# Optimization experiments

Measured on AMD Instinct MI355X. Metric: run time of the kernel, lower is better.

The kernel has to match this reference:

```python
import jax, jax.numpy as jnp
import numpy as np


def setup_inputs() -> dict:
    key = jax.random.key(0)
    ks = jax.random.split(key, 4)
    B, T, D, U = 32, 1024, 1024, 1024
    x = jax.random.normal(ks[0], (B, T, D), dtype=jnp.float32)
    W = jax.random.normal(ks[1], (D, 4 * U), dtype=jnp.float32) * (1.0 / np.sqrt(D))
    b = jnp.zeros((4 * U,), dtype=jnp.float32)
    Vr = jax.random.normal(ks[2], (U,), dtype=jnp.float32) * 0.1
    Vf = jax.random.normal(ks[3], (U,), dtype=jnp.float32) * 0.1
    h0 = jnp.zeros((B, U), dtype=jnp.float32)
    c0 = jnp.zeros((B, U), dtype=jnp.float32)
    return {"x": x, "h0": h0, "c0": c0, "W": W, "b": b, "Vr": Vr, "Vf": Vf}


def _sru(x, h0, c0, W, b, Vr, Vf):
    B, T, D = x.shape
    U = Vr.shape[0]
    # Batched matmul across all timesteps, then sequential elementwise scan.
    g = jnp.einsum('btd,dk->btk', x, W) + b            # [B, T, 4U]
    g = jnp.moveaxis(g, 1, 0)                          # [T, B, 4U]
    g1, g2, g3, g4 = jnp.split(g, 4, axis=-1)          # each [T, B, U]

    def step(c_, gs):
        a1, a2, a3, a4 = gs
        f = jax.nn.sigmoid(a1 + Vf * c_)
        c = f * c_ + (1.0 - f) * a2
        r = jax.nn.sigmoid(a3 + Vr * c_)
        h = r * c + (1.0 - r) * a4
        return c, h

    c_last, hs = jax.lax.scan(step, c0, (g1, g2, g3, g4))
    return jnp.moveaxis(hs, 0, 1)                      # [B, T, U]


def reference(x, h0, c0, W, b, Vr, Vf):
    return _sru(x, h0, c0, W, b, Vr, Vf)
```

## Files before the change

### kernel.cpp

```cpp
#include <hip/hip_runtime.h>
#include <cstdint>
#include <cstddef>

typedef short short8 __attribute__((ext_vector_type(8)));
typedef short s16x4 __attribute__((ext_vector_type(4)));
typedef float f32x4 __attribute__((ext_vector_type(4)));

typedef const __attribute__((address_space(1))) void* gas_ptr;
typedef __attribute__((address_space(3))) void* las_ptr;

__device__ __forceinline__ unsigned short f2bf(float f) {
    unsigned int u = __float_as_uint(f);
    u += 0x7fffu + ((u >> 16) & 1u);
    return (unsigned short)(u >> 16);
}
__device__ __forceinline__ float bf2f(unsigned short s) {
    return __uint_as_float(((unsigned int)s) << 16);
}
__device__ __forceinline__ float sigmoid_f(float z) {
    return __builtin_amdgcn_rcpf(1.0f + __expf(-z));
}
__device__ __forceinline__ void async_copy16(const void* gp, void* lp) {
    __builtin_amdgcn_global_load_lds((gas_ptr)gp, (las_ptr)lp, 16, 0, 0);
}

__global__ __launch_bounds__(256) void cvt_x_kernel(const float* __restrict__ in,
                                                    unsigned short* __restrict__ out) {
    size_t i = ((size_t)blockIdx.x * 256 + threadIdx.x) * 8;
    float4 v0 = *(const float4*)(in + i);
    float4 v1 = *(const float4*)(in + i + 4);
    short8 o;
    o[0]=(short)f2bf(v0.x); o[1]=(short)f2bf(v0.y); o[2]=(short)f2bf(v0.z); o[3]=(short)f2bf(v0.w);
    o[4]=(short)f2bf(v1.x); o[5]=(short)f2bf(v1.y); o[6]=(short)f2bf(v1.z); o[7]=(short)f2bf(v1.w);
    *(short8*)(out + i) = o;
}

__global__ __launch_bounds__(256) void cvt_w_kernel(const float* __restrict__ W,
                                                    unsigned short* __restrict__ Wt) {
    __shared__ unsigned short tile[64][65];
    int bk = blockIdx.x >> 6, bn = blockIdx.x & 63;
    int k0 = bk * 64, n0 = bn * 64;
    int t = threadIdx.x;
    int cr = t >> 6;
    int cc = t & 63;
#pragma unroll
    for (int i = 0; i < 16; ++i) {
        int row = i * 4 + cr;
        tile[row][cc] = f2bf(W[(size_t)(k0 + row) * 4096 + n0 + cc]);
    }
    __syncthreads();
#pragma unroll
    for (int i = 0; i < 16; ++i) {
        int nrow = i * 4 + cr;
        Wt[(size_t)(n0 + nrow) * 1024 + k0 + cc] = tile[cc][nrow];
    }
}

__global__ __launch_bounds__(256, 2) void gemm_kernel(const unsigned short* __restrict__ A,
                                                      const unsigned short* __restrict__ Bt,
                                                      const float* __restrict__ bias,
                                                      unsigned short* __restrict__ gT) {
    __shared__ __align__(16) unsigned short As[128 * 64];
    __shared__ __align__(16) unsigned short Bs[128 * 64];

    int bid = blockIdx.x;
    int band = bid >> 8;
    int r = bid & 255;
    int mt = band * 8 + (r >> 5);
    int nt = r & 31;
    int m0 = mt * 128, n0 = nt * 128;

    int tidx = threadIdx.x;
    int lane = tidx & 63, wv = tidx >> 6;
    int wm = wv >> 1, wn = wv & 1;
    int l15 = lane & 15, quad = lane >> 4;

    f32x4 acc[4][4] = {};

    for (int k0 = 0; k0 < 1024; k0 += 64) {
        __syncthreads();
#pragma unroll
        for (int i = 0; i < 4; ++i) {
            int ci = (wv * 4 + i) * 64 + lane;
            int row = ci >> 3, cc = ci & 7;
            int sc = (cc ^ (row & 7)) << 3;
            const unsigned short* ga = A + (size_t)(m0 + row) * 1024 + k0 + sc;
            async_copy16(ga, (char*)As + (wv * 4 + i) * 1024);
            const unsigned short* gb = Bt + (size_t)(n0 + row) * 1024 + k0 + sc;
            async_copy16(gb, (char*)Bs + (wv * 4 + i) * 1024);
        }
        __syncthreads();
#pragma unroll
        for (int kt = 0; kt < 2; ++kt) {
            short8 af[4], bf[4];
#pragma unroll
            for (int mt2 = 0; mt2 < 4; ++mt2) {
                int row = wm * 64 + mt2 * 16 + l15;
                int kc = kt * 4 + quad;
                af[mt2] = *(const short8*)((const char*)As + row * 128 + ((kc ^ (row & 7)) << 4));
            }
#pragma unroll
            for (int nt2 = 0; nt2 < 4; ++nt2) {
                int rown = wn * 64 + nt2 * 16 + l15;
                int kc = kt * 4 + quad;
                bf[nt2] = *(const short8*)((const char*)Bs + rown * 128 + ((kc ^ (rown & 7)) << 4));
            }
#pragma unroll
            for (int mt2 = 0; mt2 < 4; ++mt2)
#pragma unroll
                for (int nt2 = 0; nt2 < 4; ++nt2)
                    acc[mt2][nt2] = __builtin_amdgcn_mfma_f32_16x16x32_bf16(
                        af[mt2], bf[nt2], acc[mt2][nt2], 0, 0, 0);
        }
    }

#pragma unroll
    for (int mt2 = 0; mt2 < 4; ++mt2) {
        int mbase = m0 + wm * 64 + mt2 * 16 + quad * 4;
        int b_ = mbase >> 10, t_ = mbase & 1023;
#pragma unroll
        for (int nt2 = 0; nt2 < 4; ++nt2) {
            int n = n0 + wn * 64 + nt2 * 16 + l15;
            int gate = n >> 10, u = n & 1023;
            float bv = bias[n];
            s16x4 pk;
            pk[0] = (short)f2bf(acc[mt2][nt2][0] + bv);
            pk[1] = (short)f2bf(acc[mt2][nt2][1] + bv);
            pk[2] = (short)f2bf(acc[mt2][nt2][2] + bv);
            pk[3] = (short)f2bf(acc[mt2][nt2][3] + bv);
            size_t off = ((((size_t)(t_ >> 3) * 32 + (size_t)b_) * 4 + (size_t)gate) << 13)
                         + ((size_t)u << 3) + (size_t)(t_ & 7);
            *(s16x4*)(gT + off) = pk;
        }
    }
}

__global__ __launch_bounds__(128) void scan_kernel(const unsigned short* __restrict__ gT,
                                                   const float* __restrict__ c0,
                                                   const float* __restrict__ Vr,
                                                   const float* __restrict__ Vf,
                                                   float* __restrict__ h) {
    __shared__ __align__(16) unsigned short sbuf[8 * 2048];

    const int NT = 128;
    const int D = 8;
    int blk = blockIdx.x;
    int b = blk >> 4;
    int u0 = (blk & 15) << 6;
    int tid = threadIdx.x;
    int wv = tid >> 6;
    int lane = tid & 63;

    if (wv == 0) {
        size_t base = ((size_t)b * 4) * 8192 + ((size_t)(u0 + lane) << 3);
        const unsigned short* pg0 = gT + base;
        const unsigned short* pg1 = pg0 + 8192;
        const unsigned short* pg2 = pg1 + 8192;
        const unsigned short* pg3 = pg2 + 8192;
#pragma unroll
        for (int g = 0; g < D - 1; ++g) {
            char* ld = (char*)sbuf + (g & 7) * 4096;
            size_t o = (size_t)g << 20;
            async_copy16(pg0 + o, ld);
            async_copy16(pg1 + o, ld + 1024);
            async_copy16(pg2 + o, ld + 2048);
            async_copy16(pg3 + o, ld + 3072);
        }
        for (int j = 0; j < NT; ++j) {
            if (j < NT - (D - 2)) {
                asm volatile("s_waitcnt vmcnt(24)" ::: "memory");
            } else {
                asm volatile("s_waitcnt vmcnt(0)" ::: "memory");
            }
            __builtin_amdgcn_s_barrier();
            int g = j + D - 1;
            if (g < NT) {
                char* ld = (char*)sbuf + (g & 7) * 4096;
                size_t o = (size_t)g << 20;
                async_copy16(pg0 + o, ld);
                async_copy16(pg1 + o, ld + 1024);
                async_copy16(pg2 + o, ld + 2048);
                async_copy16(pg3 + o, ld + 3072);
            }
        }
    } else {
        int u = u0 + lane;
        float c = c0[(b << 10) + u];
        float vf = Vf[u], vr = Vr[u];
        float* hb = h + ((size_t)b << 20) + u;
        const unsigned short* ls = sbuf + (size_t)lane * 8;
        for (int j = 0; j < NT; ++j) {
            __builtin_amdgcn_s_barrier();
            asm volatile("" ::: "memory");
            int so = (j & 7) * 2048;
            short8 a1 = *(const short8*)(ls + so);
            short8 a2 = *(const short8*)(ls + so + 512);
            short8 a3 = *(const short8*)(ls + so + 1024);
            short8 a4 = *(const short8*)(ls + so + 1536);
            int t0 = j * 8;
#pragma unroll
            for (int i = 0; i < 8; ++i) {
                float x1 = bf2f((unsigned short)a1[i]);
                float x2 = bf2f((unsigned short)a2[i]);
                float x3 = bf2f((unsigned short)a3[i]);
                float x4 = bf2f((unsigned short)a4[i]);
                float f  = sigmoid_f(x1 + vf * c);
                float cn = fmaf(f, c - x2, x2);
                float rr = sigmoid_f(x3 + vr * c);
                float hv = fmaf(rr, cn - x4, x4);
                c = cn;
                hb[(size_t)(t0 + i) << 10] = hv;
            }
        }
    }
}

extern "C" void kernel_launch(void* const* d_in, const int* in_sizes, int n_in,
                              void* d_out, int out_size, void* d_ws, size_t ws_size,
                              hipStream_t stream) {
    const float* x  = (const float*)d_in[0];
    const float* c0 = (const float*)d_in[2];
    const float* W  = (const float*)d_in[3];
    const float* b  = (const float*)d_in[4];
    const float* Vr = (const float*)d_in[5];
    const float* Vf = (const float*)d_in[6];
    float* h = (float*)d_out;

    char* ws = (char*)d_ws;
    unsigned short* xb = (unsigned short*)ws;
    unsigned short* wt = (unsigned short*)(ws + (size_t)67108864);
    unsigned short* gT = (unsigned short*)(ws + (size_t)75497472);

    cvt_x_kernel<<<16384, 256, 0, stream>>>(x, xb);
    cvt_w_kernel<<<1024, 256, 0, stream>>>(W, wt);
    gemm_kernel<<<8192, 256, 0, stream>>>(xb, wt, b, gT);
    scan_kernel<<<512, 128, 0, stream>>>(gT, c0, Vr, Vf, h);
}
```

Before: 550.3 us.

## Split scan into serial c-checkpoint pass and parallel h-recompute pass

The sequential scan now runs only the cell-state recurrence, reading just the forget and candidate gates, and stores a checkpoint of c every 128 timesteps into reused workspace. A second kernel launches one thread per (chunk, batch, unit), starts from those checkpoints, and recomputes c alongside h for its 128-step chunk, streaming all four gates directly from global memory with register prefetch. This moves the h computation and output writes off the latency-bound serial path and spreads them across many more threads. The cost is an extra launch, rereading gates 1 and 2, and the serial pass stopping after 112 of 128 blocks because the last chunk needs no checkpoint.

```diff
diff --git a/kernel.cpp b/kernel.cpp
--- a/kernel.cpp
+++ b/kernel.cpp
@@ -135,14 +135,13 @@
     }
 }
 
-__global__ __launch_bounds__(128) void scan_kernel(const unsigned short* __restrict__ gT,
-                                                   const float* __restrict__ c0,
-                                                   const float* __restrict__ Vr,
-                                                   const float* __restrict__ Vf,
-                                                   float* __restrict__ h) {
-    __shared__ __align__(16) unsigned short sbuf[8 * 2048];
-
-    const int NT = 128;
+__global__ __launch_bounds__(128) void scan_c_kernel(const unsigned short* __restrict__ gT,
+                                                     const float* __restrict__ c0,
+                                                     const float* __restrict__ Vf,
+                                                     float* __restrict__ cB) {
+    __shared__ __align__(16) unsigned short sbuf[8 * 1024];
+
+    const int NT = 112;
     const int D = 8;
     int blk = blockIdx.x;
     int b = blk >> 4;
@@ -155,62 +154,97 @@
         size_t base = ((size_t)b * 4) * 8192 + ((size_t)(u0 + lane) << 3);
         const unsigned short* pg0 = gT + base;
         const unsigned short* pg1 = pg0 + 8192;
-        const unsigned short* pg2 = pg1 + 8192;
-        const unsigned short* pg3 = pg2 + 8192;
 #pragma unroll
         for (int g = 0; g < D - 1; ++g) {
-            char* ld = (char*)sbuf + (g & 7) * 4096;
+            char* ld = (char*)sbuf + (g & 7) * 2048;
             size_t o = (size_t)g << 20;
             async_copy16(pg0 + o, ld);
             async_copy16(pg1 + o, ld + 1024);
-            async_copy16(pg2 + o, ld + 2048);
-            async_copy16(pg3 + o, ld + 3072);
         }
         for (int j = 0; j < NT; ++j) {
             if (j < NT - (D - 2)) {
-                asm volatile("s_waitcnt vmcnt(24)" ::: "memory");
+                asm volatile("s_waitcnt vmcnt(12)" ::: "memory");
             } else {
                 asm volatile("s_waitcnt vmcnt(0)" ::: "memory");
             }
             __builtin_amdgcn_s_barrier();
             int g = j + D - 1;
             if (g < NT) {
-                char* ld = (char*)sbuf + (g & 7) * 4096;
+                char* ld = (char*)sbuf + (g & 7) * 2048;
                 size_t o = (size_t)g << 20;
                 async_copy16(pg0 + o, ld);
                 async_copy16(pg1 + o, ld + 1024);
-                async_copy16(pg2 + o, ld + 2048);
-                async_copy16(pg3 + o, ld + 3072);
             }
         }
     } else {
         int u = u0 + lane;
         float c = c0[(b << 10) + u];
-        float vf = Vf[u], vr = Vr[u];
-        float* hb = h + ((size_t)b << 20) + u;
+        float vf = Vf[u];
         const unsigned short* ls = sbuf + (size_t)lane * 8;
         for (int j = 0; j < NT; ++j) {
             __builtin_amdgcn_s_barrier();
             asm volatile("" ::: "memory");
-            int so = (j & 7) * 2048;
+            int so = (j & 7) * 1024;
             short8 a1 = *(const short8*)(ls + so);
             short8 a2 = *(const short8*)(ls + so + 512);
-            short8 a3 = *(const short8*)(ls + so + 1024);
-            short8 a4 = *(const short8*)(ls + so + 1536);
-            int t0 = j * 8;
 #pragma unroll
             for (int i = 0; i < 8; ++i) {
                 float x1 = bf2f((unsigned short)a1[i]);
                 float x2 = bf2f((unsigned short)a2[i]);
-                float x3 = bf2f((unsigned short)a3[i]);
-                float x4 = bf2f((unsigned short)a4[i]);
                 float f  = sigmoid_f(x1 + vf * c);
-                float cn = fmaf(f, c - x2, x2);
-                float rr = sigmoid_f(x3 + vr * c);
-                float hv = fmaf(rr, cn - x4, x4);
-                c = cn;
-                hb[(size_t)(t0 + i) << 10] = hv;
-            }
+                c = fmaf(f, c - x2, x2);
+            }
+            if ((j & 15) == 15) {
+                cB[((size_t)(j >> 4) << 15) + (size_t)(b << 10) + u] = c;
+            }
+        }
+    }
+}
+
+__global__ __launch_bounds__(256) void scan_h_kernel(const unsigned short* __restrict__ gT,
+                                                     const float* __restrict__ c0,
+                                                     const float* __restrict__ cB,
+                                                     const float* __restrict__ Vr,
+                                                     const float* __restrict__ Vf,
+                                                     float* __restrict__ h) {
+    int idx = blockIdx.x * 256 + threadIdx.x;
+    int u = idx & 1023;
+    int rb = idx >> 10;
+    int r = rb >> 5, b = rb & 31;
+    float vf = Vf[u], vr = Vr[u];
+    float c = (r == 0) ? c0[(b << 10) + u]
+                       : cB[((size_t)(r - 1) << 15) + (size_t)(b << 10) + u];
+    const unsigned short* base = gT + ((size_t)b * 4) * 8192 + ((size_t)u << 3);
+    float* hb = h + ((size_t)b << 20) + u;
+    int tb0 = r << 4;
+
+    const unsigned short* p0 = base + ((size_t)tb0 << 20);
+    short8 n1 = *(const short8*)(p0);
+    short8 n2 = *(const short8*)(p0 + 8192);
+    short8 n3 = *(const short8*)(p0 + 16384);
+    short8 n4 = *(const short8*)(p0 + 24576);
+    for (int j = 0; j < 16; ++j) {
+        short8 a1 = n1, a2 = n2, a3 = n3, a4 = n4;
+        if (j < 15) {
+            const unsigned short* q = base + ((size_t)(tb0 + j + 1) << 20);
+            n1 = *(const short8*)(q);
+            n2 = *(const short8*)(q + 8192);
+            n3 = *(const short8*)(q + 16384);
+            n4 = *(const short8*)(q + 24576);
+        }
+        int t0 = (tb0 + j) * 8;
+#pragma unroll
+        for (int i = 0; i < 8; ++i) {
+            float x1 = bf2f((unsigned short)a1[i]);
+            float x2 = bf2f((unsigned short)a2[i]);
+            float x3 = bf2f((unsigned short)a3[i]);
+            float x4 = bf2f((unsigned short)a4[i]);
+            float f  = sigmoid_f(x1 + vf * c);
+            float cp = c;
+            c = fmaf(f, c - x2, x2);
+            float rr = sigmoid_f(x3 + vr * cp);
+            float hv = fmaf(rr, c - x4, x4);
+            hb[(size_t)(t0 + i) << 10] = hv;
         }
     }
 }
@@ -230,9 +264,11 @@
     unsigned short* xb = (unsigned short*)ws;
     unsigned short* wt = (unsigned short*)(ws + (size_t)67108864);
     unsigned short* gT = (unsigned short*)(ws + (size_t)75497472);
+    float* cB = (float*)ws;
 
     cvt_x_kernel<<<16384, 256, 0, stream>>>(x, xb);
     cvt_w_kernel<<<1024, 256, 0, stream>>>(W, wt);
     gemm_kernel<<<8192, 256, 0, stream>>>(xb, wt, b, gT);
-    scan_kernel<<<512, 128, 0, stream>>>(gT, c0, Vr, Vf, h);
-}
+    scan_c_kernel<<<512, 128, 0, stream>>>(gT, c0, Vf, cB);
+    scan_h_kernel<<<1024, 256, 0, stream>>>(gT, c0, cB, Vr, Vf, h);
+}
```

Result: slower. 582.8 us (+5.9%).
